# Performance work log

Measured on AMD Instinct MI355X. Metric: run time of the kernel, lower is better.

Reference implementation:

```python
import jax, jax.numpy as jnp
import numpy as np

N_NODES = 100000
N_EDGES = 1600000
IN_CH = 128
OUT_CH = 32
HEADS = 4
NEG_SLOPE = 0.2


def setup_inputs() -> dict:
    key = jax.random.key(0)
    k1, k2, k3, k4 = jax.random.split(key, 4)
    x = jax.random.normal(k1, (N_NODES, IN_CH), dtype=jnp.float32)
    # xavier-ish scale for params
    weight = jax.random.normal(k2, (IN_CH, HEADS * OUT_CH), dtype=jnp.float32) * 0.1
    att = jax.random.normal(k3, (1, HEADS, 2 * OUT_CH), dtype=jnp.float32) * 0.1
    edge_index = jax.random.randint(k4, (2, N_EDGES), 0, N_NODES, dtype=jnp.int64)
    return {"x": x, "weight": weight, "att": att, "edge_index": edge_index}


def reference(x, weight, att, edge_index):
    num_nodes = x.shape[0]
    # project and split heads: [N, H, C]
    h = jnp.matmul(x, weight).reshape(num_nodes, HEADS, OUT_CH)
    row, col = edge_index[0], edge_index[1]
    x_i = h[row]   # [E, H, C]
    x_j = h[col]   # [E, H, C]
    # alpha_e = sum_c att[:, :, :C]*x_i + att[:, :, C:]*x_j  -> [E, H]
    a_i = att[0, :, :OUT_CH]   # [H, C]
    a_j = att[0, :, OUT_CH:]   # [H, C]
    alpha = jnp.einsum('ehc,hc->eh', x_i, a_i) + jnp.einsum('ehc,hc->eh', x_j, a_j)
    alpha = jnp.where(alpha >= 0, alpha, NEG_SLOPE * alpha)  # leaky_relu
    # segment softmax over destination node (col)
    amax = jax.ops.segment_max(alpha, col, num_segments=num_nodes)  # [N, H]
    amax = jnp.where(jnp.isfinite(amax), amax, 0.0)  # empty segments -> 0
    e = jnp.exp(alpha - amax[col])
    s = jax.ops.segment_sum(e, col, num_segments=num_nodes)  # [N, H]
    alpha = e / (s[col] + 1e-16)
    # weighted aggregation: scatter-add x_j * alpha to destination nodes
    msg = x_j * alpha[:, :, None]  # [E, H, C]
    out = jax.ops.segment_sum(msg, col, num_segments=num_nodes)  # [N, H, C]
    # concat=True
    return out.reshape(num_nodes, HEADS * OUT_CH)
```

## Files before the change

### kernel.cpp

```cpp
#include <hip/hip_runtime.h>
#include <hip/hip_bf16.h>

#define N_NODES 100000
#define N_EDGES 1600000
#define K_DIM 128
#define N_DIM 128
#define BM_WORDS 3125
#define PART_STRIDE 3136
#define FLAG_BLOCKS 256
#define PART_OFF 4096
#define BROWS 64

typedef __attribute__((ext_vector_type(8))) short bf16x8;
typedef __attribute__((ext_vector_type(4))) float f32x4;

__device__ inline unsigned short f2bf(float f) {
    __hip_bfloat16 b = __float2bfloat16(f);
    return __builtin_bit_cast(unsigned short, b);
}

__global__ __launch_bounds__(256)
void flag_partial(const int* __restrict__ ei, unsigned int* __restrict__ parts) {
    __shared__ unsigned int lbm[BM_WORDS];
    for (int i = threadIdx.x; i < BM_WORDS; i += 256) lbm[i] = 0;
    __syncthreads();

    bool is64 = ((ei[1] | ei[3] | ei[5] | ei[7]) == 0);
    const int base = blockIdx.x * (N_EDGES / FLAG_BLOCKS);
    if (is64) {
        const uint4* p = (const uint4*)(ei + 2 * N_EDGES + 2 * base);
        for (int t = threadIdx.x; t < 3125; t += 256) {
            uint4 v = p[t];
            atomicOr(&lbm[v.x >> 5], 1u << (v.x & 31));
            atomicOr(&lbm[v.z >> 5], 1u << (v.z & 31));
        }
    } else {
        const uint2* p = (const uint2*)(ei + N_EDGES + base);
        for (int t = threadIdx.x; t < 3125; t += 256) {
            uint2 v = p[t];
            atomicOr(&lbm[v.x >> 5], 1u << (v.x & 31));
            atomicOr(&lbm[v.y >> 5], 1u << (v.y & 31));
        }
    }
    __syncthreads();

    unsigned int* dst = parts + (size_t)blockIdx.x * PART_STRIDE;
    for (int i = threadIdx.x; i < BM_WORDS; i += 256) dst[i] = lbm[i];
}

__global__ __launch_bounds__(256, 3)
void gemm_fused(const float* __restrict__ xf,
                const float* __restrict__ wf,
                const unsigned int* __restrict__ parts,
                float* __restrict__ out) {
    __shared__ __attribute__((aligned(16))) unsigned short ldsW[N_DIM * 128];
    __shared__ __attribute__((aligned(16))) unsigned short ldsA[BROWS * 128];
    __shared__ unsigned int lmask[4][2];

    const int tid  = threadIdx.x;
    const int lane = tid & 63;
    const int wave = tid >> 6;
    const int rb0  = blockIdx.x * BROWS;

    {
        const unsigned int* p =
            parts + (size_t)tid * PART_STRIDE + blockIdx.x * 2;
        uint2 pv = *(const uint2*)p;
#pragma unroll
        for (int off = 32; off; off >>= 1) {
            pv.x |= __shfl_xor(pv.x, off);
            pv.y |= __shfl_xor(pv.y, off);
        }
        if (lane == 0) { lmask[wave][0] = pv.x; lmask[wave][1] = pv.y; }
    }

#pragma unroll
    for (int i = 0; i < 8; ++i) {
        int c  = i * 256 + tid;
        int n  = c & 127;
        int k0 = (c >> 7) << 3;
        unsigned short tmp[8];
#pragma unroll
        for (int j = 0; j < 8; ++j) tmp[j] = f2bf(wf[(k0 + j) * N_DIM + n]);
        int byte = n * 256 + k0 * 2;
        byte ^= (n & 7) << 4;
        *(uint4*)((char*)ldsW + byte) = *(const uint4*)tmp;
    }

#pragma unroll
    for (int i = 0; i < 4; ++i) {
        int c  = i * 256 + tid;
        int rl = c >> 4;
        int k8 = c & 15;
        int rg = rb0 + rl;
        if (rg >= N_NODES) rg = N_NODES - 1;
        f32x4 v0 = *(const f32x4*)(xf + (size_t)rg * K_DIM + k8 * 8);
        f32x4 v1 = *(const f32x4*)(xf + (size_t)rg * K_DIM + k8 * 8 + 4);
        unsigned short t8[8];
#pragma unroll
        for (int j = 0; j < 4; ++j) {
            t8[j]     = f2bf(v0[j]);
            t8[4 + j] = f2bf(v1[j]);
        }
        int byte = rl * 256 + k8 * 16;
        byte ^= (rl & 7) << 4;
        *(uint4*)((char*)ldsA + byte) = *(const uint4*)t8;
    }
    __syncthreads();

    const int m    = lane & 15;
    const int quad = lane >> 4;
    const int arow = wave * 16 + m;

    f32x4 acc[8];
#pragma unroll
    for (int t = 0; t < 8; ++t) acc[t] = (f32x4){0.f, 0.f, 0.f, 0.f};

#pragma unroll
    for (int kk = 0; kk < 4; ++kk) {
        const int kbase = kk * 32 + quad * 8;
        int abyte = (arow * 128 + kbase) * 2;
        abyte ^= (arow & 7) << 4;
        bf16x8 af = *(const bf16x8*)((const char*)ldsA + abyte);
#pragma unroll
        for (int t = 0; t < 8; ++t) {
            int bn = t * 16 + m;
            int bbyte = (bn * 128 + kbase) * 2;
            bbyte ^= (bn & 7) << 4;
            bf16x8 bfrag = *(const bf16x8*)((const char*)ldsW + bbyte);
            acc[t] = __builtin_amdgcn_mfma_f32_16x16x32_bf16(af, bfrag, acc[t], 0, 0, 0);
        }
    }

    const unsigned int fm0 = lmask[0][0] | lmask[1][0] | lmask[2][0] | lmask[3][0];
    const unsigned int fm1 = lmask[0][1] | lmask[1][1] | lmask[2][1] | lmask[3][1];

#pragma unroll
    for (int r = 0; r < 4; ++r) {
        int lrow = wave * 16 + quad * 4 + r;
        int orow = rb0 + lrow;
        if (orow < N_NODES) {
            unsigned int w = (lrow & 32) ? fm1 : fm0;
            float fmul = ((w >> (lrow & 31)) & 1) ? 1.0f : 0.0f;
#pragma unroll
            for (int t = 0; t < 8; ++t)
                out[(size_t)orow * N_DIM + t * 16 + m] = acc[t][r] * fmul;
        }
    }
}

extern "C" void kernel_launch(void* const* d_in, const int* in_sizes, int n_in,
                              void* d_out, int out_size, void* d_ws, size_t ws_size,
                              hipStream_t stream) {
    const float* x = (const float*)d_in[0];
    const float* w = (const float*)d_in[1];
    const int* ei = (const int*)d_in[3];
    float* out = (float*)d_out;

    unsigned int* parts = (unsigned int*)d_ws + PART_OFF;

    flag_partial<<<FLAG_BLOCKS, 256, 0, stream>>>(ei, parts);
    gemm_fused<<<(N_NODES + BROWS - 1) / BROWS, 256, 0, stream>>>(x, w, parts, out);
}
```

Baseline: 121.6 us.

## Precompute swizzled bf16 weight image once and stream it into LDS directly

Moves the fp32-to-bf16 conversion and swizzle of the weight matrix into the first kernel, run once by 16 blocks, writing a packed image to workspace. The GEMM blocks then copy that image straight into LDS with `global_load_lds`, instead of each block doing strided fp32 loads and conversions. The x-row loads are also hoisted to the start of the kernel so they overlap with the weight copy and the mask reduction. This adds a workspace dependency between the two kernels and relies on the direct-to-LDS loads completing before the barrier.

Result: no change. 120.8 us, median of 2 (-0.7%).

```diff
diff --git a/kernel.cpp b/kernel.cpp
--- a/kernel.cpp
+++ b/kernel.cpp
@@ -8,7 +8,8 @@
 #define BM_WORDS 3125
 #define PART_STRIDE 3136
 #define FLAG_BLOCKS 256
-#define PART_OFF 4096
+#define WIMG_WORDS 8192
+#define PART_OFF 8192
 #define BROWS 64
 
 typedef __attribute__((ext_vector_type(8))) short bf16x8;
@@ -20,8 +21,22 @@
 }
 
 __global__ __launch_bounds__(256)
-void flag_partial(const int* __restrict__ ei, unsigned int* __restrict__ parts) {
+void flag_partial(const int* __restrict__ ei, const float* __restrict__ wf,
+                  unsigned int* __restrict__ wimg,
+                  unsigned int* __restrict__ parts) {
     __shared__ unsigned int lbm[BM_WORDS];
+
+    if (blockIdx.x < 16 && threadIdx.x < 128) {
+        int g  = blockIdx.x * 128 + threadIdx.x;
+        int n  = g >> 4;
+        int k0 = (g & 15) << 3;
+        unsigned short tmp[8];
+#pragma unroll
+        for (int j = 0; j < 8; ++j) tmp[j] = f2bf(wf[(k0 + j) * N_DIM + n]);
+        int byte = (n * 256 + k0 * 2) ^ ((n & 7) << 4);
+        *(uint4*)((char*)wimg + byte) = *(const uint4*)tmp;
+    }
+
     for (int i = threadIdx.x; i < BM_WORDS; i += 256) lbm[i] = 0;
     __syncthreads();
 
@@ -50,7 +65,7 @@
 
 __global__ __launch_bounds__(256, 3)
 void gemm_fused(const float* __restrict__ xf,
-                const float* __restrict__ wf,
+                const unsigned int* __restrict__ wimg,
                 const unsigned int* __restrict__ parts,
                 float* __restrict__ out) {
     __shared__ __attribute__((aligned(16))) unsigned short ldsW[N_DIM * 128];
@@ -61,6 +76,29 @@
     const int lane = tid & 63;
     const int wave = tid >> 6;
     const int rb0  = blockIdx.x * BROWS;
+
+    f32x4 av[4][2];
+#pragma unroll
+    for (int i = 0; i < 4; ++i) {
+        int c  = i * 256 + tid;
+        int rl = c >> 4;
+        int k8 = c & 15;
+        int rg = rb0 + rl;
+        if (rg >= N_NODES) rg = N_NODES - 1;
+        av[i][0] = *(const f32x4*)(xf + (size_t)rg * K_DIM + k8 * 8);
+        av[i][1] = *(const f32x4*)(xf + (size_t)rg * K_DIM + k8 * 8 + 4);
+    }
+
+#pragma unroll
+    for (int i = 0; i < 8; ++i) {
+        int off = i * 4096 + wave * 1024;
+        __builtin_amdgcn_global_load_lds(
+            (const __attribute__((address_space(1))) unsigned int*)
+                ((const char*)wimg + off + lane * 16),
+            (__attribute__((address_space(3))) unsigned int*)
+                ((char*)ldsW + off),
+            16, 0, 0);
+    }
 
     {
         const unsigned int* p =
@@ -75,35 +113,17 @@
     }
 
 #pragma unroll
-    for (int i = 0; i < 8; ++i) {
-        int c  = i * 256 + tid;
-        int n  = c & 127;
-        int k0 = (c >> 7) << 3;
-        unsigned short tmp[8];
-#pragma unroll
-        for (int j = 0; j < 8; ++j) tmp[j] = f2bf(wf[(k0 + j) * N_DIM + n]);
-        int byte = n * 256 + k0 * 2;
-        byte ^= (n & 7) << 4;
-        *(uint4*)((char*)ldsW + byte) = *(const uint4*)tmp;
-    }
-
-#pragma unroll
     for (int i = 0; i < 4; ++i) {
         int c  = i * 256 + tid;
         int rl = c >> 4;
         int k8 = c & 15;
-        int rg = rb0 + rl;
-        if (rg >= N_NODES) rg = N_NODES - 1;
-        f32x4 v0 = *(const f32x4*)(xf + (size_t)rg * K_DIM + k8 * 8);
-        f32x4 v1 = *(const f32x4*)(xf + (size_t)rg * K_DIM + k8 * 8 + 4);
         unsigned short t8[8];
 #pragma unroll
         for (int j = 0; j < 4; ++j) {
-            t8[j]     = f2bf(v0[j]);
-            t8[4 + j] = f2bf(v1[j]);
+            t8[j]     = f2bf(av[i][0][j]);
+            t8[4 + j] = f2bf(av[i][1][j]);
         }
-        int byte = rl * 256 + k8 * 16;
-        byte ^= (rl & 7) << 4;
+        int byte = (rl * 256 + k8 * 16) ^ ((rl & 7) << 4);
         *(uint4*)((char*)ldsA + byte) = *(const uint4*)t8;
     }
     __syncthreads();
@@ -119,14 +139,12 @@
 #pragma unroll
     for (int kk = 0; kk < 4; ++kk) {
         const int kbase = kk * 32 + quad * 8;
-        int abyte = (arow * 128 + kbase) * 2;
-        abyte ^= (arow & 7) << 4;
+        int abyte = (arow * 256 + kbase * 2) ^ ((arow & 7) << 4);
         bf16x8 af = *(const bf16x8*)((const char*)ldsA + abyte);
 #pragma unroll
         for (int t = 0; t < 8; ++t) {
             int bn = t * 16 + m;
-            int bbyte = (bn * 128 + kbase) * 2;
-            bbyte ^= (bn & 7) << 4;
+            int bbyte = (bn * 256 + kbase * 2) ^ ((bn & 7) << 4);
             bf16x8 bfrag = *(const bf16x8*)((const char*)ldsW + bbyte);
             acc[t] = __builtin_amdgcn_mfma_f32_16x16x32_bf16(af, bfrag, acc[t], 0, 0, 0);
         }
@@ -157,8 +175,9 @@
     const int* ei = (const int*)d_in[3];
     float* out = (float*)d_out;
 
+    unsigned int* wimg  = (unsigned int*)d_ws;
     unsigned int* parts = (unsigned int*)d_ws + PART_OFF;
 
-    flag_partial<<<FLAG_BLOCKS, 256, 0, stream>>>(ei, parts);
-    gemm_fused<<<(N_NODES + BROWS - 1) / BROWS, 256, 0, stream>>>(x, w, parts, out);
+    flag_partial<<<FLAG_BLOCKS, 256, 0, stream>>>(ei, w, wimg, parts);
+    gemm_fused<<<(N_NODES + BROWS - 1) / BROWS, 256, 0, stream>>>(x, wimg, parts, out);
 }
```
